# Kernel tuning notes

Measured on AMD Instinct MI355X. Metric: run time of the kernel, lower is better.

## Reference

```python
import jax, jax.numpy as jnp
import numpy as np

L = 16384   # nodes (rows)
E = 131072  # edges
SP = 20000  # column positions (nodes + periodic images)
C = 512     # embed_dim
H = 8       # heads
DH = C // H # head dim = 64
HID = 1024  # ffn hidden


def setup_inputs() -> dict:
    key = jax.random.key(0)
    ks = jax.random.split(key, 16)
    p = lambda k, shape: jax.random.normal(k, shape, dtype=jnp.float32) * 0.02
    return dict(
        x=jax.random.normal(ks[0], (L, C), dtype=jnp.float32),
        row_index=jax.random.randint(ks[1], (E,), 0, L),
        col_index=jax.random.randint(ks[2], (E,), 0, L),
        to_col_index=jax.random.randint(ks[3], (E,), 0, SP),
        att_bias=jax.random.normal(ks[4], (E, H), dtype=jnp.float32),
        pos_att_bias=jax.random.normal(ks[5], (E, H), dtype=jnp.float32),
        dist=jax.random.uniform(ks[6], (E,), minval=0.5, maxval=5.0),
        pos=jax.random.normal(ks[7], (L, 3), dtype=jnp.float32),
        col_pos=jax.random.normal(ks[8], (SP, 3), dtype=jnp.float32),
        ln1_g=jnp.ones((C,), jnp.float32), ln1_b=jnp.zeros((C,), jnp.float32),
        ln2_g=jnp.ones((C,), jnp.float32), ln2_b=jnp.zeros((C,), jnp.float32),
        Wq=p(ks[9], (C, C)), bq=jnp.zeros((C,), jnp.float32),
        Wk=p(ks[10], (C, C)), bk=jnp.zeros((C,), jnp.float32),
        Wv=p(ks[11], (C, C)), bv=jnp.zeros((C,), jnp.float32),
        Wvec=p(ks[12], (3, C)), bvec=jnp.zeros((C,), jnp.float32),
        Wo=p(ks[13], (C, C)), bo=jnp.zeros((C,), jnp.float32),
        W1=p(ks[14], (C, HID)), b1=jnp.zeros((HID,), jnp.float32),
        W2=p(ks[15], (HID, C)), b2=jnp.zeros((C,), jnp.float32),
    )


def _ln(x, g, b, eps=1e-5):
    mu = jnp.mean(x, -1, keepdims=True)
    v = jnp.mean((x - mu) ** 2, -1, keepdims=True)
    return (x - mu) * jax.lax.rsqrt(v + eps) * g + b


def reference(x, row_index, col_index, to_col_index, att_bias, pos_att_bias,
              dist, pos, col_pos, ln1_g, ln1_b, ln2_g, ln2_b,
              Wq, bq, Wk, bk, Wv, bv, Wvec, bvec, Wo, bo, W1, b1, W2, b2):
    Lx = x.shape[0]
    # --- pre-norm + Euclidean sparse attention ---
    z = _ln(x, ln1_g, ln1_b)
    q = (z @ Wq + bq).reshape(Lx, H, DH)
    k = (z @ Wk + bk).reshape(Lx, H, DH)
    v = (z @ Wv + bv).reshape(Lx, H, DH)
    qe = q[row_index]          # (E,H,DH) gather
    ke = k[col_index]          # (E,H,DH)
    ve = v[col_index]          # (E,H,DH)
    # relative unit direction from receiving node to (PBC-shifted) column node
    rel = (col_pos[to_col_index] - pos[row_index]) / dist[:, None]   # (E,3)
    ve = ve + (rel @ Wvec + bvec).reshape(-1, H, DH)
    # Euclidean (negative squared L2) attention score + positional bias
    score = -jnp.sum((qe - ke) ** 2, axis=-1) / np.float32(np.sqrt(DH)) + pos_att_bias  # (E,H)
    # segment softmax over edges grouped by row_index
    m = jax.ops.segment_max(score, row_index, num_segments=Lx)       # (L,H)
    m = jnp.where(jnp.isfinite(m), m, 0.0)
    pexp = jnp.exp(score - m[row_index])
    den = jax.ops.segment_sum(pexp, row_index, num_segments=Lx)      # (L,H)
    deng = den[row_index]
    alpha = pexp / jnp.where(deng == 0.0, 1.0, deng)                 # (E,H)
    out = jax.ops.segment_sum(alpha[:, :, None] * ve, row_index, num_segments=Lx)
    att = out.reshape(Lx, C) @ Wo + bo
    x = x + att
    # --- pre-norm + feed-forward ---
    z2 = _ln(x, ln2_g, ln2_b)
    ff = jax.nn.gelu(z2 @ W1 + b1) @ W2 + b2
    return x + ff
```

## Files before the change

kernel.cpp:

```cpp
#include <hip/hip_runtime.h>

#define L_NODES 16384
#define E_EDGES 131072
#define CDIM 512
#define QKVDIM 1536
#define HEADS 8
#define DHEAD 64
#define HID 1024

typedef __attribute__((ext_vector_type(8))) short bf16x8;
typedef __attribute__((ext_vector_type(4))) float f32x4;

__device__ inline unsigned short f2b(float f) {
    union { float f; unsigned int u; } v{f};
    unsigned int r = (v.u + 0x7fffu + ((v.u >> 16) & 1u)) >> 16;
    return (unsigned short)r;
}
__device__ inline float b2f(unsigned short h) {
    union { unsigned int u; float f; } v;
    v.u = (unsigned int)h << 16;
    return v.f;
}

__device__ inline void async_lds16(const void* g, void* l) {
    __builtin_amdgcn_global_load_lds(
        (const __attribute__((address_space(1))) unsigned int*)g,
        (__attribute__((address_space(3))) unsigned int*)l,
        16, 0, 0);
}

__global__ __launch_bounds__(256) void ln_bf16_kernel(
    const float* __restrict__ x, const float* __restrict__ g,
    const float* __restrict__ b, short* __restrict__ out)
{
    int row = blockIdx.x;
    int t = threadIdx.x;
    const float2* xr = (const float2*)(x + (size_t)row * CDIM);
    float2 v = xr[t];
    float s = v.x + v.y;
    float sq = v.x * v.x + v.y * v.y;
    for (int off = 32; off; off >>= 1) {
        s += __shfl_xor(s, off);
        sq += __shfl_xor(sq, off);
    }
    __shared__ float ss[4], sqs[4];
    int wave = t >> 6, lane = t & 63;
    if (lane == 0) { ss[wave] = s; sqs[wave] = sq; }
    __syncthreads();
    s = ss[0] + ss[1] + ss[2] + ss[3];
    sq = sqs[0] + sqs[1] + sqs[2] + sqs[3];
    float mu = s * (1.0f / CDIM);
    float var = sq * (1.0f / CDIM) - mu * mu;
    float inv = rsqrtf(var + 1e-5f);
    int c = t * 2;
    unsigned short h0 = f2b((v.x - mu) * inv * g[c] + b[c]);
    unsigned short h1 = f2b((v.y - mu) * inv * g[c + 1] + b[c + 1]);
    unsigned int packed = ((unsigned int)h1 << 16) | h0;
    *(unsigned int*)(out + (size_t)row * CDIM + c) = packed;
}

__global__ __launch_bounds__(256) void prep_kernel(
    const float* __restrict__ Wq, const float* __restrict__ Wk,
    const float* __restrict__ Wv, const float* __restrict__ Wo,
    const float* __restrict__ W1, const float* __restrict__ W2,
    short* __restrict__ wqkvT, short* __restrict__ woT,
    short* __restrict__ w1T, short* __restrict__ w2T,
    const float* __restrict__ bq, const float* __restrict__ bk,
    const float* __restrict__ bv, float* __restrict__ bqkv,
    int* __restrict__ cnt)
{
    int bid = blockIdx.x;
    if (bid >= 2054) {
        cnt[(bid - 2054) * 256 + threadIdx.x] = 0;
        return;
    }
    if (bid >= 2048) {
        int i = (bid - 2048) * 256 + threadIdx.x;
        float val = (i < CDIM) ? bq[i] : (i < 2 * CDIM) ? bk[i - CDIM] : bv[i - 2 * CDIM];
        bqkv[i] = val;
        return;
    }
    const float* W; short* WT; int K, N, tn, tk;
    if (bid < 1024) {
        int w = bid >> 8, local = bid & 255;
        tn = local & 15; tk = local >> 4; K = 512; N = 512;
        W = (w == 0) ? Wq : (w == 1) ? Wk : (w == 2) ? Wv : Wo;
        WT = (w == 3) ? woT : wqkvT + (size_t)w * 512 * 512;
    } else if (bid < 1536) {
        int local = bid - 1024;
        tn = local & 31; tk = local >> 5; K = 512; N = 1024;
        W = W1; WT = w1T;
    } else {
        int local = bid - 1536;
        tn = local & 15; tk = local >> 4; K = 1024; N = 512;
        W = W2; WT = w2T;
    }
    __shared__ float tile[32][33];
    int tx = threadIdx.x & 31, ty = threadIdx.x >> 5;
    int n0 = tn * 32, k0 = tk * 32;
#pragma unroll
    for (int r = 0; r < 4; r++)
        tile[ty + r * 8][tx] = W[(size_t)(k0 + ty + r * 8) * N + n0 + tx];
    __syncthreads();
#pragma unroll
    for (int r = 0; r < 4; r++)
        WT[(size_t)(n0 + ty + r * 8) * K + k0 + tx] = f2b(tile[tx][ty + r * 8]);
}

__global__ __launch_bounds__(256) void gemm_bf16_kernel(
    const short* __restrict__ A, const short* __restrict__ B,
    const float* __restrict__ bias, const float* __restrict__ res,
    float* __restrict__ outf, short* __restrict__ outb,
    int M, int N, int K, int act)
{
    __shared__ short As[128 * 32];
    __shared__ short Bs[128 * 32];
    int t = threadIdx.x;
    int bm = blockIdx.y * 128, bn = blockIdx.x * 128;
    int wave = t >> 6, lane = t & 63;
    int wm = (wave & 1) * 64, wn = (wave >> 1) * 64;
    int crow = lane & 15, quad = lane >> 4;

    f32x4 acc[4][4] = {};

    for (int k0 = 0; k0 < K; k0 += 32) {
#pragma unroll
        for (int c = 0; c < 2; c++) {
            int idx = c * 256 + t;
            int row = idx >> 2, chunk = idx & 3;
            async_lds16(A + (size_t)(bm + row) * K + k0 + chunk * 8,
                        (char*)As + c * 4096 + wave * 1024 + lane * 16);
            async_lds16(B + (size_t)(bn + row) * K + k0 + chunk * 8,
                        (char*)Bs + c * 4096 + wave * 1024 + lane * 16);
        }
        __syncthreads();
        bf16x8 af[4], bg[4];
#pragma unroll
        for (int i = 0; i < 4; i++)
            af[i] = *(const bf16x8*)&As[(wm + i * 16 + crow) * 32 + quad * 8];
#pragma unroll
        for (int j = 0; j < 4; j++)
            bg[j] = *(const bf16x8*)&Bs[(wn + j * 16 + crow) * 32 + quad * 8];
#pragma unroll
        for (int i = 0; i < 4; i++)
#pragma unroll
            for (int j = 0; j < 4; j++)
                acc[i][j] = __builtin_amdgcn_mfma_f32_16x16x32_bf16(af[i], bg[j], acc[i][j], 0, 0, 0);
        __syncthreads();
    }

#pragma unroll
    for (int i = 0; i < 4; i++) {
#pragma unroll
        for (int j = 0; j < 4; j++) {
            int n = bn + wn + j * 16 + crow;
            float bi = bias ? bias[n] : 0.0f;
#pragma unroll
            for (int r = 0; r < 4; r++) {
                int mrow = bm + wm + i * 16 + quad * 4 + r;
                float val = acc[i][j][r] + bi;
                if (act) {
                    float u = 0.7978845608028654f * (val + 0.044715f * val * val * val);
                    val = 0.5f * val * (1.0f + tanhf(u));
                }
                if (res) val += res[(size_t)mrow * N + n];
                if (outf) outf[(size_t)mrow * N + n] = val;
                if (outb) outb[(size_t)mrow * N + n] = f2b(val);
            }
        }
    }
}

__global__ void hist_kernel(const int* __restrict__ row_index, int* __restrict__ cnt)
{
    int e = blockIdx.x * 256 + threadIdx.x;
    if (e < E_EDGES) atomicAdd(&cnt[row_index[e]], 1);
}

__global__ void scan_kernel(const int* __restrict__ cnt, int* __restrict__ row_start,
                            int* __restrict__ cursor)
{
    int t = threadIdx.x;
    const int PER = L_NODES / 64;
    int local = 0;
    for (int i = 0; i < PER; i++) local += cnt[t * PER + i];
    int v = local;
    for (int off = 1; off < 64; off <<= 1) {
        int u = __shfl_up(v, off);
        if (t >= off) v += u;
    }
    int run = v - local;
    for (int i = 0; i < PER; i++) {
        row_start[t * PER + i] = run;
        cursor[t * PER + i] = run;
        run += cnt[t * PER + i];
    }
    if (t == 63) row_start[L_NODES] = run;
}

__global__ void scatter_kernel(const int* __restrict__ row_index, const int* __restrict__ col_index,
                               const int* __restrict__ to_col_index, const float* __restrict__ dist,
                               const float* __restrict__ pos, const float* __restrict__ col_pos,
                               const float* __restrict__ pos_att_bias,
                               int* __restrict__ cursor, int4* __restrict__ emeta,
                               float* __restrict__ pabp)
{
    int e = blockIdx.x * 256 + threadIdx.x;
    if (e < E_EDGES) {
        int row = row_index[e];
        int p = atomicAdd(&cursor[row], 1);
        int tci = to_col_index[e];
        float dinv = 1.0f / dist[e];
        float r0 = (col_pos[tci * 3]     - pos[row * 3])     * dinv;
        float r1 = (col_pos[tci * 3 + 1] - pos[row * 3 + 1]) * dinv;
        float r2 = (col_pos[tci * 3 + 2] - pos[row * 3 + 2]) * dinv;
        emeta[p] = make_int4(col_index[e], __float_as_int(r0), __float_as_int(r1),
                             __float_as_int(r2));
        const float4* pb = (const float4*)(pos_att_bias + (size_t)e * HEADS);
        float4 b0 = pb[0], b1 = pb[1];
        float4* dst = (float4*)(pabp + (size_t)p * HEADS);
        dst[0] = b0; dst[1] = b1;
    }
}

__global__ __launch_bounds__(512) void attn_kernel(
    const short* __restrict__ qkv, const int4* __restrict__ emeta,
    const float* __restrict__ pabp, const int* __restrict__ row_start,
    const float* __restrict__ Wvec, const float* __restrict__ bvec,
    short* __restrict__ out_bf)
{
    int r = blockIdx.x;
    int t = threadIdx.x;
    int h = t >> 6, lane = t & 63;
    int es = lane >> 3, ch = lane & 7;
    int cbase = h * DHEAD + ch * 8;

    float qv[8], wv0[8], wv1[8], wv2[8], bvv[8];
    {
        bf16x8 qh = *(const bf16x8*)(qkv + (size_t)r * QKVDIM + cbase);
#pragma unroll
        for (int j = 0; j < 8; j++) qv[j] = b2f((unsigned short)qh[j]);
        float4 a0 = *(const float4*)(Wvec + cbase);
        float4 a1 = *(const float4*)(Wvec + cbase + 4);
        float4 b0 = *(const float4*)(Wvec + CDIM + cbase);
        float4 b1 = *(const float4*)(Wvec + CDIM + cbase + 4);
        float4 c0 = *(const float4*)(Wvec + 2 * CDIM + cbase);
        float4 c1 = *(const float4*)(Wvec + 2 * CDIM + cbase + 4);
        float4 d0 = *(const float4*)(bvec + cbase);
        float4 d1 = *(const float4*)(bvec + cbase + 4);
        wv0[0]=a0.x; wv0[1]=a0.y; wv0[2]=a0.z; wv0[3]=a0.w; wv0[4]=a1.x; wv0[5]=a1.y; wv0[6]=a1.z; wv0[7]=a1.w;
        wv1[0]=b0.x; wv1[1]=b0.y; wv1[2]=b0.z; wv1[3]=b0.w; wv1[4]=b1.x; wv1[5]=b1.y; wv1[6]=b1.z; wv1[7]=b1.w;
        wv2[0]=c0.x; wv2[1]=c0.y; wv2[2]=c0.z; wv2[3]=c0.w; wv2[4]=c1.x; wv2[5]=c1.y; wv2[6]=c1.z; wv2[7]=c1.w;
        bvv[0]=d0.x; bvv[1]=d0.y; bvv[2]=d0.z; bvv[3]=d0.w; bvv[4]=d1.x; bvv[5]=d1.y; bvv[6]=d1.z; bvv[7]=d1.w;
    }

    int e0 = row_start[r], e1 = row_start[r + 1];
    float m = -1e30f, l = 0.0f;
    float acc[8] = {};

    for (int idx = e0; idx < e1; idx += 8) {
        int myidx = idx + es;
        bool act = myidx < e1;
        int cidx = act ? myidx : (e1 - 1);
        int4 em = emeta[cidx];
        float pab = pabp[(size_t)cidx * HEADS + h];
        const short* kp = qkv + (size_t)em.x * QKVDIM + CDIM + cbase;
        bf16x8 k8 = *(const bf16x8*)kp;
        bf16x8 v8 = *(const bf16x8*)(kp + CDIM);
        float s = 0.0f;
        float vf[8];
#pragma unroll
        for (int j = 0; j < 8; j++) {
            float kf = b2f((unsigned short)k8[j]);
            vf[j] = b2f((unsigned short)v8[j]);
            float d = qv[j] - kf;
            s = fmaf(d, d, s);
        }
        s += __shfl_xor(s, 1);
        s += __shfl_xor(s, 2);
        s += __shfl_xor(s, 4);
        float score = act ? (-s * 0.125f + pab) : -1e30f;
        float bmax = score;
        bmax = fmaxf(bmax, __shfl_xor(bmax, 8));
        bmax = fmaxf(bmax, __shfl_xor(bmax, 16));
        bmax = fmaxf(bmax, __shfl_xor(bmax, 32));
        float mn = fmaxf(m, bmax);
        float scale = __expf(m - mn);
        float pexp = __expf(score - mn);
        m = mn;
        l = l * scale + pexp;
        float r0 = __int_as_float(em.y), r1 = __int_as_float(em.z), r2 = __int_as_float(em.w);
#pragma unroll
        for (int j = 0; j < 8; j++) {
            float vv = vf[j] + r0 * wv0[j] + r1 * wv1[j] + r2 * wv2[j] + bvv[j];
            acc[j] = acc[j] * scale + pexp * vv;
        }
    }
    l += __shfl_xor(l, 8); l += __shfl_xor(l, 16); l += __shfl_xor(l, 32);
#pragma unroll
    for (int j = 0; j < 8; j++) {
        acc[j] += __shfl_xor(acc[j], 8);
        acc[j] += __shfl_xor(acc[j], 16);
        acc[j] += __shfl_xor(acc[j], 32);
    }
    float inv = (l > 0.0f) ? 1.0f / l : 0.0f;
    if (es == 0) {
        bf16x8 o;
#pragma unroll
        for (int j = 0; j < 8; j++) o[j] = (short)f2b(acc[j] * inv);
        *(bf16x8*)(out_bf + (size_t)r * CDIM + cbase) = o;
    }
}

extern "C" void kernel_launch(void* const* d_in, const int* in_sizes, int n_in,
                              void* d_out, int out_size, void* d_ws, size_t ws_size,
                              hipStream_t stream)
{
    const float* x            = (const float*)d_in[0];
    const int*   row_index    = (const int*)d_in[1];
    const int*   col_index    = (const int*)d_in[2];
    const int*   to_col_index = (const int*)d_in[3];
    const float* pos_att_bias = (const float*)d_in[5];
    const float* dist         = (const float*)d_in[6];
    const float* pos          = (const float*)d_in[7];
    const float* col_pos      = (const float*)d_in[8];
    const float* ln1_g = (const float*)d_in[9];
    const float* ln1_b = (const float*)d_in[10];
    const float* ln2_g = (const float*)d_in[11];
    const float* ln2_b = (const float*)d_in[12];
    const float* Wq = (const float*)d_in[13];  const float* bq = (const float*)d_in[14];
    const float* Wk = (const float*)d_in[15];  const float* bk = (const float*)d_in[16];
    const float* Wv = (const float*)d_in[17];  const float* bv = (const float*)d_in[18];
    const float* Wvec = (const float*)d_in[19]; const float* bvec = (const float*)d_in[20];
    const float* Wo = (const float*)d_in[21];  const float* bo = (const float*)d_in[22];
    const float* W1 = (const float*)d_in[23];  const float* b1 = (const float*)d_in[24];
    const float* W2 = (const float*)d_in[25];  const float* b2 = (const float*)d_in[26];

    char* ws = (char*)d_ws;
    size_t off = 0;
    auto alloc = [&](size_t bytes) -> void* {
        void* p = ws + off;
        off = (off + bytes + 255) & ~(size_t)255;
        return p;
    };
    const size_t LC = (size_t)L_NODES * CDIM;
    short* qkvb = (short*)alloc((size_t)L_NODES * QKVDIM * 2);
    float* x1f  = (float*)alloc(LC * 4);
    short* zbf  = (short*)alloc(LC * 2);
    short* abf  = (short*)alloc(LC * 2);
    short* wqkvT = (short*)alloc((size_t)QKVDIM * CDIM * 2);
    short* woT   = (short*)alloc((size_t)CDIM * CDIM * 2);
    short* w1T   = (short*)alloc((size_t)CDIM * HID * 2);
    short* w2T   = (short*)alloc((size_t)HID * CDIM * 2);
    float* bqkv  = (float*)alloc(QKVDIM * 4);
    int* cnt       = (int*)alloc(L_NODES * 4);
    int* cursor    = (int*)alloc(L_NODES * 4);
    int* row_start = (int*)alloc((L_NODES + 1) * 4);
    int4* emeta    = (int4*)alloc((size_t)E_EDGES * 16);
    short* hbf = (short*)qkvb;
    float* pabp = x1f;

    prep_kernel<<<2118, 256, 0, stream>>>(Wq, Wk, Wv, Wo, W1, W2,
                                          wqkvT, woT, w1T, w2T,
                                          bq, bk, bv, bqkv, cnt);

    ln_bf16_kernel<<<L_NODES, 256, 0, stream>>>(x, ln1_g, ln1_b, zbf);

    dim3 gqkv(QKVDIM / 128, L_NODES / 128);
    gemm_bf16_kernel<<<gqkv, 256, 0, stream>>>(zbf, wqkvT, bqkv, nullptr, nullptr, qkvb,
                                               L_NODES, QKVDIM, CDIM, 0);

    hist_kernel<<<E_EDGES / 256, 256, 0, stream>>>(row_index, cnt);
    scan_kernel<<<1, 64, 0, stream>>>(cnt, row_start, cursor);
    scatter_kernel<<<E_EDGES / 256, 256, 0, stream>>>(row_index, col_index, to_col_index,
                                                      dist, pos, col_pos, pos_att_bias,
                                                      cursor, emeta, pabp);

    attn_kernel<<<L_NODES, 512, 0, stream>>>(qkvb, emeta, pabp, row_start, Wvec, bvec, abf);

    dim3 g512(CDIM / 128, L_NODES / 128);
    gemm_bf16_kernel<<<g512, 256, 0, stream>>>(abf, woT, bo, x, x1f, nullptr, L_NODES, CDIM, CDIM, 0);

    ln_bf16_kernel<<<L_NODES, 256, 0, stream>>>(x1f, ln2_g, ln2_b, zbf);

    dim3 g1024(HID / 128, L_NODES / 128);
    gemm_bf16_kernel<<<g1024, 256, 0, stream>>>(zbf, w1T, b1, nullptr, nullptr, hbf, L_NODES, HID, CDIM, 1);
    gemm_bf16_kernel<<<g512, 256, 0, stream>>>(hbf, w2T, b2, x1f, (float*)d_out, nullptr, L_NODES, CDIM, HID, 0);
}
```

Before: 507.2 us.

## Remap attention to one wavefront per row with software-prefetched edge loop

The attention kernel now gives each row a single 64-lane wavefront, packing four rows per 256-thread block. Each lane owns 8 channels of the full 512-wide row and walks that row's edges serially, so the cross-lane max and sum shuffles and the inactive-lane padding of the old 8-edges-per-iteration scheme go away. A register prefetch loads the next edge's metadata, bias and K/V vectors (and the metadata two edges ahead) while the current edge is computed, to hide gather latency. The trade-off is less memory-level parallelism per row: one edge in flight per wave instead of eight, with a longer serial loop for high-degree rows.

```diff
diff --git a/kernel.cpp b/kernel.cpp
--- a/kernel.cpp
+++ b/kernel.cpp
@@ -223,17 +223,16 @@
     }
 }
 
-__global__ __launch_bounds__(512) void attn_kernel(
+__global__ __launch_bounds__(256) void attn_kernel(
     const short* __restrict__ qkv, const int4* __restrict__ emeta,
     const float* __restrict__ pabp, const int* __restrict__ row_start,
     const float* __restrict__ Wvec, const float* __restrict__ bvec,
     short* __restrict__ out_bf)
 {
-    int r = blockIdx.x;
-    int t = threadIdx.x;
-    int h = t >> 6, lane = t & 63;
-    int es = lane >> 3, ch = lane & 7;
-    int cbase = h * DHEAD + ch * 8;
+    int lane = threadIdx.x & 63;
+    int r = blockIdx.x * 4 + (threadIdx.x >> 6);
+    int h = lane >> 3;
+    int cbase = lane * 8;
 
     float qv[8], wv0[8], wv1[8], wv2[8], bvv[8];
     {
@@ -258,15 +257,31 @@
     float m = -1e30f, l = 0.0f;
     float acc[8] = {};
 
-    for (int idx = e0; idx < e1; idx += 8) {
-        int myidx = idx + es;
-        bool act = myidx < e1;
-        int cidx = act ? myidx : (e1 - 1);
-        int4 em = emeta[cidx];
-        float pab = pabp[(size_t)cidx * HEADS + h];
-        const short* kp = qkv + (size_t)em.x * QKVDIM + CDIM + cbase;
-        bf16x8 k8 = *(const bf16x8*)kp;
-        bf16x8 v8 = *(const bf16x8*)(kp + CDIM);
+    int4 em_n, em_n2;
+    float pab_n;
+    bf16x8 k_n, v_n;
+    if (e0 < e1) {
+        em_n = emeta[e0];
+        em_n2 = emeta[(e0 + 1 < e1) ? e0 + 1 : e1 - 1];
+        pab_n = pabp[(size_t)e0 * HEADS + h];
+        const short* kp = qkv + (size_t)em_n.x * QKVDIM + CDIM + cbase;
+        k_n = *(const bf16x8*)kp;
+        v_n = *(const bf16x8*)(kp + CDIM);
+    }
+    for (int idx = e0; idx < e1; ++idx) {
+        int4 em = em_n;
+        float pab = pab_n;
+        bf16x8 k8 = k_n, v8 = v_n;
+        em_n = em_n2;
+        int i2 = (idx + 2 < e1) ? idx + 2 : e1 - 1;
+        em_n2 = emeta[i2];
+        int i1 = (idx + 1 < e1) ? idx + 1 : e1 - 1;
+        pab_n = pabp[(size_t)i1 * HEADS + h];
+        {
+            const short* kp = qkv + (size_t)em_n.x * QKVDIM + CDIM + cbase;
+            k_n = *(const bf16x8*)kp;
+            v_n = *(const bf16x8*)(kp + CDIM);
+        }
         float s = 0.0f;
         float vf[8];
 #pragma unroll
@@ -279,12 +294,8 @@
         s += __shfl_xor(s, 1);
         s += __shfl_xor(s, 2);
         s += __shfl_xor(s, 4);
-        float score = act ? (-s * 0.125f + pab) : -1e30f;
-        float bmax = score;
-        bmax = fmaxf(bmax, __shfl_xor(bmax, 8));
-        bmax = fmaxf(bmax, __shfl_xor(bmax, 16));
-        bmax = fmaxf(bmax, __shfl_xor(bmax, 32));
-        float mn = fmaxf(m, bmax);
+        float score = -s * 0.125f + pab;
+        float mn = fmaxf(m, score);
         float scale = __expf(m - mn);
         float pexp = __expf(score - mn);
         m = mn;
@@ -293,23 +304,14 @@
 #pragma unroll
         for (int j = 0; j < 8; j++) {
             float vv = vf[j] + r0 * wv0[j] + r1 * wv1[j] + r2 * wv2[j] + bvv[j];
-            acc[j] = acc[j] * scale + pexp * vv;
-        }
-    }
-    l += __shfl_xor(l, 8); l += __shfl_xor(l, 16); l += __shfl_xor(l, 32);
-#pragma unroll
-    for (int j = 0; j < 8; j++) {
-        acc[j] += __shfl_xor(acc[j], 8);
-        acc[j] += __shfl_xor(acc[j], 16);
-        acc[j] += __shfl_xor(acc[j], 32);
+            acc[j] = fmaf(acc[j], scale, pexp * vv);
+        }
     }
     float inv = (l > 0.0f) ? 1.0f / l : 0.0f;
-    if (es == 0) {
-        bf16x8 o;
-#pragma unroll
-        for (int j = 0; j < 8; j++) o[j] = (short)f2b(acc[j] * inv);
-        *(bf16x8*)(out_bf + (size_t)r * CDIM + cbase) = o;
-    }
+    bf16x8 o;
+#pragma unroll
+    for (int j = 0; j < 8; j++) o[j] = (short)f2b(acc[j] * inv);
+    *(bf16x8*)(out_bf + (size_t)r * CDIM + cbase) = o;
 }
 
 extern "C" void kernel_launch(void* const* d_in, const int* in_sizes, int n_in,
@@ -376,7 +378,7 @@
                                                       dist, pos, col_pos, pos_att_bias,
                                                       cursor, emeta, pabp);
 
-    attn_kernel<<<L_NODES, 512, 0, stream>>>(qkvb, emeta, pabp, row_start, Wvec, bvec, abf);
+    attn_kernel<<<L_NODES / 4, 256, 0, stream>>>(qkvb, emeta, pabp, row_start, Wvec, bvec, abf);
 
     dim3 g512(CDIM / 128, L_NODES / 128);
     gemm_bf16_kernel<<<g512, 256, 0, stream>>>(abf, woT, bo, x, x1f, nullptr, L_NODES, CDIM, CDIM, 0);
```

Result: faster. 442.3 us (-12.8%).
